# Kernel optimization log

Hardware: AMD Instinct MI355X
Metric: run time of the kernel (lower is better)

The kernel has to match this reference:

```python
import jax, jax.numpy as jnp
import numpy as np

NJ, NS = 30000, 12000            # num job / skill nodes
E_JS, E_SJ, E_SS = 300000, 300000, 150000
SBERT, HID, OUT = 384, 128, 128
H = 2                             # GAT heads (concat=True)
NEG_SLOPE = 0.2


def setup_inputs() -> dict:
    key = jax.random.key(0)
    ks = iter(jax.random.split(key, 64))
    nrm = lambda shape, s=1.0: jax.random.normal(next(ks), shape, jnp.float32) * s
    ridx = lambda n, hi: jax.random.randint(next(ks), (n,), 0, hi, jnp.int32)
    W = 0.05  # weight scale to keep activations sane across layers
    return dict(
        x_job=nrm((NJ, SBERT)), x_skill=nrm((NS, SBERT)),
        ei_js_src=ridx(E_JS, NJ), ei_js_dst=ridx(E_JS, NS),
        ei_sj_src=ridx(E_SJ, NS), ei_sj_dst=ridx(E_SJ, NJ),
        ei_ss_src=ridx(E_SS, NS), ei_ss_dst=ridx(E_SS, NS),
        query=nrm((SBERT,)),
        W0_job=nrm((SBERT, HID), W), b0_job=jnp.zeros((HID,), jnp.float32),
        g0_job=jnp.ones((HID,), jnp.float32), be0_job=jnp.zeros((HID,), jnp.float32),
        W0_skill=nrm((SBERT, HID), W), b0_skill=jnp.zeros((HID,), jnp.float32),
        g0_skill=jnp.ones((HID,), jnp.float32), be0_skill=jnp.zeros((HID,), jnp.float32),
        gat_Ws=nrm((2, 3, HID, H * HID), W), gat_Wd=nrm((2, 3, HID, H * HID), W),
        gat_as=nrm((2, 3, H, HID), W), gat_ad=nrm((2, 3, H, HID), W),
        gat_b=jnp.zeros((2, 3, H * HID), jnp.float32),
        inter_W=nrm((2, 2, H * HID, HID), W), inter_b=jnp.zeros((2, 2, HID), jnp.float32),
        Wjf=nrm((HID, OUT), W), bjf=jnp.zeros((OUT,), jnp.float32),
        Wq=nrm((SBERT, OUT), W), bq=jnp.zeros((OUT,), jnp.float32),
    )


def _layer_norm(x, g, b):
    mu = x.mean(-1, keepdims=True)
    var = ((x - mu) ** 2).mean(-1, keepdims=True)
    return (x - mu) * jax.lax.rsqrt(var + 1e-5) * g + b


def _gat(x_src, x_dst, src, dst, Ws, Wd, a_s, a_d, bias, num_dst):
    # PyG GATConv: lin_src/lin_dst (no bias), additive attention, scatter-softmax over dst.
    hs = (x_src @ Ws).reshape(-1, H, HID)            # [Ns,H,C]
    hd = (x_dst @ Wd).reshape(-1, H, HID)            # [Nd,H,C]
    e = jax.nn.leaky_relu((hs * a_s).sum(-1)[src] + (hd * a_d).sum(-1)[dst], NEG_SLOPE)  # [E,H]
    m = jax.ops.segment_max(e, dst, num_segments=num_dst)
    p = jnp.exp(e - m[dst])
    den = jax.ops.segment_sum(p, dst, num_segments=num_dst)
    w = p / (den[dst] + 1e-16)                       # [E,H]
    out = jax.ops.segment_sum(hs[src] * w[:, :, None], dst, num_segments=num_dst)
    return out.reshape(num_dst, H * HID) + bias


def _forward(x_job, x_skill, query,
             W0_job, b0_job, g0_job, be0_job, W0_skill, b0_skill, g0_skill, be0_skill,
             gat_Ws, gat_Wd, gat_as, gat_ad, gat_b, inter_W, inter_b, Wjf, bjf, Wq, bq,
             ei_js_src, ei_js_dst, ei_sj_src, ei_sj_dst, ei_ss_src, ei_ss_dst):
    # initial per-type lin + LN + relu (dropout = identity in eval)
    xj = jax.nn.relu(_layer_norm(x_job @ W0_job + b0_job, g0_job, be0_job))
    xs = jax.nn.relu(_layer_norm(x_skill @ W0_skill + b0_skill, g0_skill, be0_skill))
    # skill->skill relation adds self loops (src == dst node type)
    loops = jnp.arange(NS, dtype=jnp.int32)
    ss_src = jnp.concatenate([ei_ss_src, loops])
    ss_dst = jnp.concatenate([ei_ss_dst, loops])
    for i in range(2):  # num_layers
        o_s = (_gat(xj, xs, ei_js_src, ei_js_dst, gat_Ws[i, 0], gat_Wd[i, 0],
                    gat_as[i, 0], gat_ad[i, 0], gat_b[i, 0], NS)
               + _gat(xs, xs, ss_src, ss_dst, gat_Ws[i, 2], gat_Wd[i, 2],
                      gat_as[i, 2], gat_ad[i, 2], gat_b[i, 2], NS))  # HeteroConv aggr='sum'
        o_j = _gat(xs, xj, ei_sj_src, ei_sj_dst, gat_Ws[i, 1], gat_Wd[i, 1],
                   gat_as[i, 1], gat_ad[i, 1], gat_b[i, 1], NJ)
        xj = jax.nn.relu(o_j @ inter_W[i, 0] + inter_b[i, 0])
        xs = jax.nn.relu(o_s @ inter_W[i, 1] + inter_b[i, 1])
    job_emb = xj @ Wjf + bjf                          # [NJ,OUT]
    q = query @ Wq + bq                               # [OUT]
    scores = job_emb @ q                              # [NJ]
    return scores, job_emb, q


def reference(x_job, x_skill, ei_js_src, ei_js_dst, ei_sj_src, ei_sj_dst,
              ei_ss_src, ei_ss_dst, query,
              W0_job, b0_job, g0_job, be0_job, W0_skill, b0_skill, g0_skill, be0_skill,
              gat_Ws, gat_Wd, gat_as, gat_ad, gat_b, inter_W, inter_b,
              Wjf, bjf, Wq, bq):
    return _forward(x_job, x_skill, query,
                    W0_job, b0_job, g0_job, be0_job, W0_skill, b0_skill, g0_skill, be0_skill,
                    gat_Ws, gat_Wd, gat_as, gat_ad, gat_b, inter_W, inter_b, Wjf, bjf, Wq, bq,
                    ei_js_src, ei_js_dst, ei_sj_src, ei_sj_dst, ei_ss_src, ei_ss_dst)
```

## Files before the change

kernel.cpp:

```cpp
#include <hip/hip_runtime.h>
#include <hip/hip_bf16.h>
#include <math.h>

#define NJ 30000
#define NS 12000
#define E_JS 300000
#define E_SJ 300000
#define E_SS 150000
#define ETOT (E_JS + E_SJ + E_SS + NS)
#define NBINS (NS + NJ + NS)
#define NBUK ((NBINS + 63) / 64)
#define SBERT 384
#define HIST_NB 512
#define SCAT_NB 120
#define CAST_MATS 10
#define CAST_BPM 48
#define PREP_CAST (CAST_MATS * CAST_BPM)
#define PREP_WA   (PREP_CAST + 12)
#define PREP_QV   PREP_WA
#define PREP_HIST (PREP_QV + 1)

static inline int cdiv(int a, int b) { return (a + b - 1) / b; }

typedef __attribute__((ext_vector_type(8))) short bf8_t;
typedef __attribute__((ext_vector_type(4))) float f4_t;
typedef unsigned short u16;

__device__ inline float bf2f(unsigned short u) {
    union { unsigned int i; float f; } z; z.i = ((unsigned int)u) << 16; return z.f;
}
__device__ inline unsigned short f2bf(float f) {
    unsigned int x = __float_as_uint(f);
    unsigned int r = (x + 0x7fffu + ((x >> 16) & 1u)) >> 16;
    return (unsigned short)r;
}

__device__ inline void edge_decode(int e, const int* js_src, const int* js_dst,
                                   const int* sj_src, const int* sj_dst,
                                   const int* ss_src, const int* ss_dst,
                                   int& src, int& bin) {
    if (e < E_JS) { src = js_src[e]; bin = js_dst[e]; }
    else if (e < E_JS + E_SJ) { int i = e - E_JS; src = sj_src[i]; bin = NS + sj_dst[i]; }
    else if (e < E_JS + E_SJ + E_SS) { int i = e - E_JS - E_SJ; src = ss_src[i]; bin = NS + NJ + ss_dst[i]; }
    else { int i = e - E_JS - E_SJ - E_SS; src = i; bin = NS + NJ + i; }
}

struct CastT { const float* src; unsigned short* dst; int K; int N; };
struct PrepArgs {
    CastT m[CAST_MATS];
    const float* Ws; const float* as_; const float* Wd; const float* ad_;
    float* wsa; float* wda; int* bcnt;
    const float* query; const float* Wq; const float* bq; float* qv;
    const int* js_src; const int* js_dst;
    const int* sj_src; const int* sj_dst;
    const int* ss_src; const int* ss_dst;
};

__global__ __launch_bounds__(256) void k_prep(PrepArgs A) {
    __shared__ float ldt[32][33];
    __shared__ int lh[NBUK];
    int b = blockIdx.x;
    if (b < PREP_CAST) {
        int mi = b / CAST_BPM, bx = b % CAST_BPM;
        CastT cm = A.m[mi];
        int tilesN = cm.N >> 5;
        int total = (cm.K >> 5) * tilesN;
        if (bx >= total) return;
        int tk = bx / tilesN, tn = bx % tilesN;
        int k0 = tk * 32, n0 = tn * 32;
        int col = threadIdx.x & 31;
        int row0 = threadIdx.x >> 5;
#pragma unroll
        for (int r = 0; r < 4; ++r) {
            int kk = row0 + r * 8;
            ldt[kk][col] = cm.src[(size_t)(k0 + kk) * cm.N + n0 + col];
        }
        __syncthreads();
#pragma unroll
        for (int r = 0; r < 4; ++r) {
            int nn = row0 + r * 8;
            cm.dst[(size_t)(n0 + nn) * cm.K + k0 + col] = f2bf(ldt[col][nn]);
        }
    } else if (b < PREP_WA) {
        int id = (b - PREP_CAST) * 256 + threadIdx.x;
        if (id >= 2 * 1536) return;
        int which = id / 1536;
        int r = id % 1536;
        int lr = r / 256;
        int kh = r % 256;
        int k = kh / 2, h = kh % 2;
        const float* W = which ? A.Wd : A.Ws;
        const float* a = which ? A.ad_ : A.as_;
        const float* wrow = W + ((size_t)(lr * 128 + k)) * 256 + h * 128;
        const float* arow = a + (size_t)(lr * 2 + h) * 128;
        float acc = 0.f;
        for (int c2 = 0; c2 < 128; ++c2) acc += wrow[c2] * arow[c2];
        (which ? A.wda : A.wsa)[lr * 256 + k * 2 + h] = acc;
    } else if (b == PREP_QV) {
        int c = threadIdx.x;
        if (c < 128) {
            float acc = A.bq[c];
            for (int k = 0; k < SBERT; ++k) acc += A.query[k] * A.Wq[(size_t)k * 128 + c];
            A.qv[c] = acc;
        }
    } else {
        int t = threadIdx.x;
        for (int i = t; i < NBUK; i += 256) lh[i] = 0;
        __syncthreads();
        int hb = b - PREP_HIST;
        for (int e = hb * 256 + t; e < ETOT; e += HIST_NB * 256) {
            int src, bin;
            edge_decode(e, A.js_src, A.js_dst, A.sj_src, A.sj_dst, A.ss_src, A.ss_dst, src, bin);
            atomicAdd(&lh[bin >> 6], 1);
        }
        __syncthreads();
        for (int i = t; i < NBUK; i += 256) {
            int v = lh[i];
            if (v) atomicAdd(&A.bcnt[i], v);
        }
    }
}

struct GJob {
    const void* X; const unsigned short* Wt;
    const float* bias; const float* gamma; const float* beta;
    void* Y; int M; int K; int N; int ldY; int srcf32;
    const float* qv; float* sc;
    int aMode = 0;
    const float* wav0 = nullptr; const float* wav1 = nullptr;
    const float* wav2 = nullptr; const float* wav3 = nullptr;
    float* aOut = nullptr; int aStride = 0;
};
struct GPair { GJob a; GJob b; int blocksA; };

template <int EPI>
__device__ void mgemm_body(const GPair& P, int bx, int by) {
    int mb = bx;
    GJob g = (mb < P.blocksA) ? P.a : P.b;
    if (mb >= P.blocksA) mb -= P.blocksA;
    const int n0 = by * 128;
    if (n0 >= g.N) return;
    const int row0 = mb * 64;

    __shared__ __align__(16) unsigned short Al[64][40];
    __shared__ __align__(16) unsigned short Bl[128][40];
    const int t = threadIdx.x;
    const int wave = t >> 6, lane = t & 63;
    const int q = lane >> 4, c = lane & 15;
    const int K = g.K;

    f4_t acc[8];
#pragma unroll
    for (int nt = 0; nt < 8; ++nt) acc[nt] = (f4_t){0.f, 0.f, 0.f, 0.f};

    for (int k0 = 0; k0 < K; k0 += 32) {
#pragma unroll
        for (int it = 0; it < 3; ++it) {
            int idx = t + it * 256;
            int r = idx >> 2, cc = (idx & 3) * 8;
            if (r < 64) {
                int gr = row0 + r;
                if (g.srcf32) {
                    ushort4 lo = make_ushort4(0, 0, 0, 0), hi = lo;
                    if (gr < g.M) {
                        const float* Xf = (const float*)g.X;
                        const float* p = &Xf[(size_t)gr * K + k0 + cc];
                        float4 f0 = *(const float4*)p;
                        float4 f1 = *(const float4*)(p + 4);
                        lo = make_ushort4(f2bf(f0.x), f2bf(f0.y), f2bf(f0.z), f2bf(f0.w));
                        hi = make_ushort4(f2bf(f1.x), f2bf(f1.y), f2bf(f1.z), f2bf(f1.w));
                    }
                    *(ushort4*)&Al[r][cc] = lo;
                    *(ushort4*)&Al[r][cc + 4] = hi;
                } else {
                    const unsigned short* Xb = (const unsigned short*)g.X;
                    uint4 va = (gr < g.M) ? *(const uint4*)&Xb[(size_t)gr * K + k0 + cc]
                                          : make_uint4(0u, 0u, 0u, 0u);
                    *(uint4*)&Al[r][cc] = va;
                }
            } else {
                int br = r - 64;
                *(uint4*)&Bl[br][cc] = *(const uint4*)&g.Wt[(size_t)(n0 + br) * K + k0 + cc];
            }
        }
        __syncthreads();
        bf8_t af = *(const bf8_t*)&Al[wave * 16 + c][q * 8];
#pragma unroll
        for (int nt = 0; nt < 8; ++nt) {
            bf8_t bfr = *(const bf8_t*)&Bl[nt * 16 + c][q * 8];
            acc[nt] = __builtin_amdgcn_mfma_f32_16x16x32_bf16(af, bfr, acc[nt], 0, 0, 0);
        }
        __syncthreads();
    }

    float bcol[8], gcol[8], becol[8], qcol[8];
#pragma unroll
    for (int nt = 0; nt < 8; ++nt) {
        bcol[nt] = (EPI >= 1) ? g.bias[n0 + nt * 16 + c] : 0.f;
        if constexpr (EPI == 3) {
            gcol[nt] = g.gamma[nt * 16 + c];
            becol[nt] = g.beta[nt * 16 + c];
        }
        if constexpr (EPI == 1) qcol[nt] = g.qv[n0 + nt * 16 + c];
    }

#pragma unroll
    for (int r = 0; r < 4; ++r) {
        int grow = row0 + wave * 16 + q * 4 + r;
        float v[8];
#pragma unroll
        for (int nt = 0; nt < 8; ++nt) v[nt] = acc[nt][r] + bcol[nt];
        if constexpr (EPI == 3) {
            float s = 0.f, ss = 0.f;
#pragma unroll
            for (int nt = 0; nt < 8; ++nt) { s += v[nt]; ss += v[nt] * v[nt]; }
#pragma unroll
            for (int m = 8; m >= 1; m >>= 1) {
                s += __shfl_xor(s, m, 64);
                ss += __shfl_xor(ss, m, 64);
            }
            float mu = s * (1.f / 128.f);
            float var = ss * (1.f / 128.f) - mu * mu;
            float rs = rsqrtf(var + 1e-5f);
#pragma unroll
            for (int nt = 0; nt < 8; ++nt)
                v[nt] = fmaxf((v[nt] - mu) * rs * gcol[nt] + becol[nt], 0.f);
        } else if constexpr (EPI == 2) {
#pragma unroll
            for (int nt = 0; nt < 8; ++nt) v[nt] = fmaxf(v[nt], 0.f);
        }
        if constexpr (EPI == 1) {
            float part = 0.f;
#pragma unroll
            for (int nt = 0; nt < 8; ++nt) part += v[nt] * qcol[nt];
#pragma unroll
            for (int m = 8; m >= 1; m >>= 1) part += __shfl_xor(part, m, 64);
            if (c == 0 && grow < g.M) g.sc[grow] = part;
        }
        if (g.aMode > 0) {
            float pa[8];
#pragma unroll
            for (int i = 0; i < 8; ++i) pa[i] = 0.f;
#pragma unroll
            for (int nt = 0; nt < 8; ++nt) {
                int col = nt * 16 + c;
                float2 w0 = *(const float2*)&g.wav0[col * 2];
                pa[0] += v[nt] * w0.x; pa[1] += v[nt] * w0.y;
                if (g.aMode > 1) {
                    float2 w1 = *(const float2*)&g.wav1[col * 2];
                    pa[2] += v[nt] * w1.x; pa[3] += v[nt] * w1.y;
                }
                if (g.aMode > 2) {
                    float2 w2 = *(const float2*)&g.wav2[col * 2];
                    float2 w3 = *(const float2*)&g.wav3[col * 2];
                    pa[4] += v[nt] * w2.x; pa[5] += v[nt] * w2.y;
                    pa[6] += v[nt] * w3.x; pa[7] += v[nt] * w3.y;
                }
            }
#pragma unroll
            for (int m = 8; m >= 1; m >>= 1) {
                pa[0] += __shfl_xor(pa[0], m, 64); pa[1] += __shfl_xor(pa[1], m, 64);
                pa[2] += __shfl_xor(pa[2], m, 64); pa[3] += __shfl_xor(pa[3], m, 64);
                pa[4] += __shfl_xor(pa[4], m, 64); pa[5] += __shfl_xor(pa[5], m, 64);
                pa[6] += __shfl_xor(pa[6], m, 64); pa[7] += __shfl_xor(pa[7], m, 64);
            }
            if (c == 0 && grow < g.M) {
                float* ao = &g.aOut[(size_t)grow * g.aStride];
                ao[0] = pa[0]; ao[1] = pa[1];
                if (g.aMode > 1) { ao[2] = pa[2]; ao[3] = pa[3]; }
                if (g.aMode > 2) { ao[4] = pa[4]; ao[5] = pa[5]; ao[6] = pa[6]; ao[7] = pa[7]; }
            }
        }
        if (grow < g.M) {
            if constexpr (EPI == 1) {
                float* Y = (float*)g.Y;
#pragma unroll
                for (int nt = 0; nt < 8; ++nt)
                    Y[(size_t)grow * g.ldY + n0 + nt * 16 + c] = v[nt];
            } else {
                unsigned short* Y = (unsigned short*)g.Y;
#pragma unroll
                for (int nt = 0; nt < 8; ++nt)
                    Y[(size_t)grow * g.ldY + n0 + nt * 16 + c] = f2bf(v[nt]);
            }
        }
    }
}

template <int EPI>
__global__ __launch_bounds__(256) void k_mgemm(GPair P) {
    mgemm_body<EPI>(P, blockIdx.x, blockIdx.y);
}

__global__ __launch_bounds__(256) void k_lin0_scan(
    GPair P, int gemmBlocks,
    const int* __restrict__ bcnt, int* __restrict__ bukoff, int* __restrict__ bukcur) {
    if (blockIdx.x < (unsigned)gemmBlocks) {
        mgemm_body<3>(P, blockIdx.x, 0);
        return;
    }
    __shared__ int sd[256];
    int t = threadIdx.x;
    int i0 = t * 4;
    int v0 = (i0 < NBUK) ? bcnt[i0] : 0;
    int v1 = (i0 + 1 < NBUK) ? bcnt[i0 + 1] : 0;
    int v2 = (i0 + 2 < NBUK) ? bcnt[i0 + 2] : 0;
    int v3 = (i0 + 3 < NBUK) ? bcnt[i0 + 3] : 0;
    int csum = v0 + v1 + v2 + v3;
    sd[t] = csum;
    __syncthreads();
    for (int off = 1; off < 256; off <<= 1) {
        int tmp = (t >= off) ? sd[t - off] : 0;
        __syncthreads();
        sd[t] += tmp;
        __syncthreads();
    }
    int excl = sd[t] - csum;
    int p0 = excl, p1 = excl + v0, p2 = excl + v0 + v1, p3 = excl + v0 + v1 + v2;
    if (i0 < NBUK) { bukoff[i0] = p0; bukcur[i0] = p0; }
    if (i0 + 1 < NBUK) { bukoff[i0 + 1] = p1; bukcur[i0 + 1] = p1; }
    if (i0 + 2 < NBUK) { bukoff[i0 + 2] = p2; bukcur[i0 + 2] = p2; }
    if (i0 + 3 < NBUK) { bukoff[i0 + 3] = p3; bukcur[i0 + 3] = p3; }
    if (t == 0) bukoff[NBUK] = ETOT;
}

__global__ __launch_bounds__(256) void k_scatter_proj(
    GPair P, int gemmBlocks,
    const int* __restrict__ js_src, const int* __restrict__ js_dst,
    const int* __restrict__ sj_src, const int* __restrict__ sj_dst,
    const int* __restrict__ ss_src, const int* __restrict__ ss_dst,
    int* __restrict__ bukcur, uint2* __restrict__ pairs) {
    if (blockIdx.x < (unsigned)gemmBlocks) {
        mgemm_body<0>(P, blockIdx.x, blockIdx.y);
        return;
    }
    if (blockIdx.y != 0) return;
    __shared__ int lh[NBUK];
    __shared__ int lbase[NBUK];
    int t = threadIdx.x;
    int sb = blockIdx.x - gemmBlocks;
    const int CH = (ETOT + SCAT_NB - 1) / SCAT_NB;
    const int beg = sb * CH;
    const int endi = (beg + CH < ETOT) ? beg + CH : ETOT;
    for (int i = t; i < NBUK; i += 256) lh[i] = 0;
    __syncthreads();
    for (int e = beg + t; e < endi; e += 256) {
        int src, bin;
        edge_decode(e, js_src, js_dst, sj_src, sj_dst, ss_src, ss_dst, src, bin);
        atomicAdd(&lh[bin >> 6], 1);
    }
    __syncthreads();
    for (int i = t; i < NBUK; i += 256) {
        int v = lh[i];
        lbase[i] = v ? atomicAdd(&bukcur[i], v) : 0;
    }
    __syncthreads();
    for (int i = t; i < NBUK; i += 256) lh[i] = 0;
    __syncthreads();
    for (int e = beg + t; e < endi; e += 256) {
        int src, bin;
        edge_decode(e, js_src, js_dst, sj_src, sj_dst, ss_src, ss_dst, src, bin);
        int bu = bin >> 6;
        int pos = lbase[bu] + atomicAdd(&lh[bu], 1);
        pairs[pos] = make_uint2((unsigned)src, (unsigned)bin);
    }
}

__global__ __launch_bounds__(256) void k_finalize(
    const uint2* __restrict__ pairs, const int* __restrict__ bukoff,
    int* __restrict__ offs, int* __restrict__ esrc) {
    int b = blockIdx.x, t = threadIdx.x;
    int base = bukoff[b], endi = bukoff[b + 1];
    __shared__ int cnt[64], excl[64], curs[64];
    if (t < 64) cnt[t] = 0;
    __syncthreads();
    for (int i = base + t; i < endi; i += 256)
        atomicAdd(&cnt[pairs[i].y & 63], 1);
    __syncthreads();
    if (t < 64) {
        int v = cnt[t];
        int inc = v;
#pragma unroll
        for (int off = 1; off < 64; off <<= 1) {
            int tmp = __shfl_up(inc, off, 64);
            if (t >= off) inc += tmp;
        }
        excl[t] = inc - v;
        curs[t] = inc - v;
    }
    __syncthreads();
    for (int i = base + t; i < endi; i += 256) {
        uint2 p = pairs[i];
        int lb = p.y & 63;
        int pos = atomicAdd(&curs[lb], 1);
        esrc[base + pos] = (int)p.x;
    }
    if (t < 64) {
        int bin = b * 64 + t;
        if (bin < NBINS) offs[bin] = base + excl[t];
    }
    if (b == 0 && t == 0) offs[NBINS] = ETOT;
}

__device__ inline void edge_accum(
    const int* __restrict__ esrc, int beg, int endi,
    const float* __restrict__ aSrc, int sStride, int hOff, float ad,
    const unsigned short* __restrict__ hs, int hsLd, int c,
    float& ax, float& ay, float& az, float& aw, float& den) {
    for (int j = beg; j < endi; j += 4) {
        int j1 = j + 1 < endi ? j + 1 : endi - 1;
        int j2 = j + 2 < endi ? j + 2 : endi - 1;
        int j3 = j + 3 < endi ? j + 3 : endi - 1;
        int s0 = esrc[j], s1 = esrc[j1], s2 = esrc[j2], s3 = esrc[j3];
        float as0 = aSrc[(size_t)s0 * sStride + hOff];
        float as1 = aSrc[(size_t)s1 * sStride + hOff];
        float as2 = aSrc[(size_t)s2 * sStride + hOff];
        float as3 = aSrc[(size_t)s3 * sStride + hOff];
        ushort4 v0 = *(const ushort4*)&hs[(size_t)s0 * hsLd + c];
        ushort4 v1 = *(const ushort4*)&hs[(size_t)s1 * hsLd + c];
        ushort4 v2 = *(const ushort4*)&hs[(size_t)s2 * hsLd + c];
        ushort4 v3 = *(const ushort4*)&hs[(size_t)s3 * hsLd + c];
        float e0 = as0 + ad; e0 = e0 > 0.f ? e0 : 0.2f * e0;
        float e1 = as1 + ad; e1 = e1 > 0.f ? e1 : 0.2f * e1;
        float e2 = as2 + ad; e2 = e2 > 0.f ? e2 : 0.2f * e2;
        float e3 = as3 + ad; e3 = e3 > 0.f ? e3 : 0.2f * e3;
        float p0 = __expf(e0);
        float p1 = (j + 1 < endi) ? __expf(e1) : 0.f;
        float p2 = (j + 2 < endi) ? __expf(e2) : 0.f;
        float p3 = (j + 3 < endi) ? __expf(e3) : 0.f;
        ax += p0 * bf2f(v0.x) + p1 * bf2f(v1.x) + p2 * bf2f(v2.x) + p3 * bf2f(v3.x);
        ay += p0 * bf2f(v0.y) + p1 * bf2f(v1.y) + p2 * bf2f(v2.y) + p3 * bf2f(v3.y);
        az += p0 * bf2f(v0.z) + p1 * bf2f(v1.z) + p2 * bf2f(v2.z) + p3 * bf2f(v3.z);
        aw += p0 * bf2f(v0.w) + p1 * bf2f(v1.w) + p2 * bf2f(v2.w) + p3 * bf2f(v3.w);
        den += p0 + p1 + p2 + p3;
    }
}

__global__ __launch_bounds__(256) void k_gather_all(
    const int* __restrict__ offs, const int* __restrict__ esrc,
    const float* __restrict__ aJ, const float* __restrict__ aS,
    const unsigned short* __restrict__ hs1,
    const unsigned short* __restrict__ hsss, int ssLd,
    const unsigned short* __restrict__ hsj, int sjLd,
    const float* __restrict__ gb,
    unsigned short* __restrict__ oj, unsigned short* __restrict__ os,
    int jobOnly) {
    int wave = threadIdx.x >> 6, lane = threadIdx.x & 63;
    int idx = blockIdx.x * 4 + wave;
    int c = lane * 4;
    int h = (c >= 128) ? 1 : 0;
    if (jobOnly) {
        if (idx >= NJ) return;
        int d = idx;
        float ax = 0.f, ay = 0.f, az = 0.f, aw = 0.f, den = 0.f;
        int bb = NS + d;
        edge_accum(esrc, offs[bb], offs[bb + 1], aS, 8, 4 + h, aJ[(size_t)d * 4 + 2 + h],
                   hsj, sjLd, c, ax, ay, az, aw, den);
        float sc = 1.f / (den + 1e-16f);
        float4 b4 = *(const float4*)&gb[256 + c];
        float o0 = ax * sc + b4.x, o1 = ay * sc + b4.y;
        float o2 = az * sc + b4.z, o3 = aw * sc + b4.w;
        ushort4 o; o.x = f2bf(o0); o.y = f2bf(o1); o.z = f2bf(o2); o.w = f2bf(o3);
        *(ushort4*)&oj[(size_t)d * 256 + c] = o;
        return;
    }
    if (idx < NS) {
        int d = idx;
        float axA = 0.f, ayA = 0.f, azA = 0.f, awA = 0.f, denA = 0.f;
        edge_accum(esrc, offs[d], offs[d + 1], aJ, 4, h, aS[(size_t)d * 8 + 2 + h],
                   hs1, 256, c, axA, ayA, azA, awA, denA);
        float axB = 0.f, ayB = 0.f, azB = 0.f, awB = 0.f, denB = 0.f;
        int bb = NS + NJ + d;
        edge_accum(esrc, offs[bb], offs[bb + 1], aS, 8, h, aS[(size_t)d * 8 + 6 + h],
                   hsss, ssLd, c, axB, ayB, azB, awB, denB);
        float scA = 1.f / (denA + 1e-16f);
        float scB = 1.f / (denB + 1e-16f);
        float4 bA = *(const float4*)&gb[c];
        float4 bB = *(const float4*)&gb[512 + c];
        float o0 = axA * scA + bA.x + axB * scB + bB.x;
        float o1 = ayA * scA + bA.y + ayB * scB + bB.y;
        float o2 = azA * scA + bA.z + azB * scB + bB.z;
        float o3 = awA * scA + bA.w + awB * scB + bB.w;
        ushort4 o; o.x = f2bf(o0); o.y = f2bf(o1); o.z = f2bf(o2); o.w = f2bf(o3);
        *(ushort4*)&os[(size_t)d * 256 + c] = o;
    } else if (idx < NS + NJ) {
        int d = idx - NS;
        float ax = 0.f, ay = 0.f, az = 0.f, aw = 0.f, den = 0.f;
        int bb = NS + d;
        edge_accum(esrc, offs[bb], offs[bb + 1], aS, 8, 4 + h, aJ[(size_t)d * 4 + 2 + h],
                   hsj, sjLd, c, ax, ay, az, aw, den);
        float sc = 1.f / (den + 1e-16f);
        float4 b4 = *(const float4*)&gb[256 + c];
        float o0 = ax * sc + b4.x, o1 = ay * sc + b4.y;
        float o2 = az * sc + b4.z, o3 = aw * sc + b4.w;
        ushort4 o; o.x = f2bf(o0); o.y = f2bf(o1); o.z = f2bf(o2); o.w = f2bf(o3);
        *(ushort4*)&oj[(size_t)d * 256 + c] = o;
    }
}

struct FJob {
    const unsigned short* X; const unsigned short* Wt1; const float* bias1;
    int M; int K1;
    const float* wa; float* aOut; int aStride;
    const unsigned short* Wt2; const float* bias2; int N2;
    void* Y2; int ldY2; int y2f32;
    const float* qv; float* sc;
};
struct FPair { FJob a; FJob b; int blocksA; };

__global__ __launch_bounds__(256) void k_fused2(FPair P) {
    int mb = blockIdx.x;
    FJob g = (mb < P.blocksA) ? P.a : P.b;
    if (mb >= P.blocksA) mb -= P.blocksA;
    const int row0 = mb * 64;

    __shared__ __align__(16) unsigned short Al[64][40];
    __shared__ __align__(16) unsigned short Bl[128][40];
    __shared__ __align__(16) unsigned short Y1l[4][64][40];
    const int t = threadIdx.x;
    const int wave = t >> 6, lane = t & 63;
    const int q = lane >> 4, c = lane & 15;

    f4_t acc[8];
#pragma unroll
    for (int nt = 0; nt < 8; ++nt) acc[nt] = (f4_t){0.f, 0.f, 0.f, 0.f};

    for (int k0 = 0; k0 < g.K1; k0 += 32) {
#pragma unroll
        for (int it = 0; it < 3; ++it) {
            int idx = t + it * 256;
            int r = idx >> 2, cc = (idx & 3) * 8;
            if (r < 64) {
                int gr = row0 + r;
                uint4 va = (gr < g.M) ? *(const uint4*)&g.X[(size_t)gr * g.K1 + k0 + cc]
                                      : make_uint4(0u, 0u, 0u, 0u);
                *(uint4*)&Al[r][cc] = va;
            } else {
                int br = r - 64;
                *(uint4*)&Bl[br][cc] = *(const uint4*)&g.Wt1[(size_t)br * g.K1 + k0 + cc];
            }
        }
        __syncthreads();
        bf8_t af = *(const bf8_t*)&Al[wave * 16 + c][q * 8];
#pragma unroll
        for (int nt = 0; nt < 8; ++nt) {
            bf8_t bfr = *(const bf8_t*)&Bl[nt * 16 + c][q * 8];
            acc[nt] = __builtin_amdgcn_mfma_f32_16x16x32_bf16(af, bfr, acc[nt], 0, 0, 0);
        }
        __syncthreads();
    }

    float bcol[8];
#pragma unroll
    for (int nt = 0; nt < 8; ++nt) bcol[nt] = g.bias1[nt * 16 + c];
#pragma unroll
    for (int r = 0; r < 4; ++r) {
        int row = wave * 16 + q * 4 + r;
        int grow = row0 + row;
        float v[8];
#pragma unroll
        for (int nt = 0; nt < 8; ++nt) v[nt] = fmaxf(acc[nt][r] + bcol[nt], 0.f);
        if (g.wa) {
            float pa0 = 0.f, pa1 = 0.f;
#pragma unroll
            for (int nt = 0; nt < 8; ++nt) {
                float2 w0 = *(const float2*)&g.wa[(nt * 16 + c) * 2];
                pa0 += v[nt] * w0.x; pa1 += v[nt] * w0.y;
            }
#pragma unroll
            for (int m = 8; m >= 1; m >>= 1) {
                pa0 += __shfl_xor(pa0, m, 64);
                pa1 += __shfl_xor(pa1, m, 64);
            }
            if (c == 0 && grow < g.M) {
                g.aOut[(size_t)grow * g.aStride + 0] = pa0;
                g.aOut[(size_t)grow * g.aStride + 1] = pa1;
            }
        }
#pragma unroll
        for (int nt = 0; nt < 8; ++nt)
            Y1l[nt >> 1][row][(nt & 1) * 16 + c] = f2bf(v[nt]);
    }
    if (g.N2 == 0) return;
    __syncthreads();

    for (int n2 = 0; n2 < g.N2; n2 += 128) {
        f4_t acc2[8];
#pragma unroll
        for (int nt = 0; nt < 8; ++nt) acc2[nt] = (f4_t){0.f, 0.f, 0.f, 0.f};
        for (int k0 = 0; k0 < 128; k0 += 32) {
#pragma unroll
            for (int it = 0; it < 2; ++it) {
                int idx = t + it * 256;
                int br = idx >> 2, cc = (idx & 3) * 8;
                *(uint4*)&Bl[br][cc] = *(const uint4*)&g.Wt2[(size_t)(n2 + br) * 128 + k0 + cc];
            }
            __syncthreads();
            bf8_t af = *(const bf8_t*)&Y1l[k0 >> 5][wave * 16 + c][q * 8];
#pragma unroll
            for (int nt = 0; nt < 8; ++nt) {
                bf8_t bfr = *(const bf8_t*)&Bl[nt * 16 + c][q * 8];
                acc2[nt] = __builtin_amdgcn_mfma_f32_16x16x32_bf16(af, bfr, acc2[nt], 0, 0, 0);
            }
            __syncthreads();
        }
        float b2[8], qcol[8];
#pragma unroll
        for (int nt = 0; nt < 8; ++nt) {
            b2[nt] = g.bias2 ? g.bias2[n2 + nt * 16 + c] : 0.f;
            if (g.y2f32) qcol[nt] = g.qv[n2 + nt * 16 + c];
        }
#pragma unroll
        for (int r = 0; r < 4; ++r) {
            int grow = row0 + wave * 16 + q * 4 + r;
            float v[8];
#pragma unroll
            for (int nt = 0; nt < 8; ++nt) v[nt] = acc2[nt][r] + b2[nt];
            if (g.y2f32) {
                float part = 0.f;
#pragma unroll
                for (int nt = 0; nt < 8; ++nt) part += v[nt] * qcol[nt];
#pragma unroll
                for (int m = 8; m >= 1; m >>= 1) part += __shfl_xor(part, m, 64);
                if (c == 0 && grow < g.M) g.sc[grow] = part;
                if (grow < g.M) {
                    float* Y = (float*)g.Y2;
#pragma unroll
                    for (int nt = 0; nt < 8; ++nt)
                        Y[(size_t)grow * g.ldY2 + n2 + nt * 16 + c] = v[nt];
                }
            } else if (grow < g.M) {
                unsigned short* Y = (unsigned short*)g.Y2;
#pragma unroll
                for (int nt = 0; nt < 8; ++nt)
                    Y[(size_t)grow * g.ldY2 + n2 + nt * 16 + c] = f2bf(v[nt]);
            }
        }
    }
}

extern "C" void kernel_launch(void* const* d_in, const int* in_sizes, int n_in,
                              void* d_out, int out_size, void* d_ws, size_t ws_size,
                              hipStream_t stream) {
    const float* x_job   = (const float*)d_in[0];
    const float* x_skill = (const float*)d_in[1];
    const int* js_src = (const int*)d_in[2];
    const int* js_dst = (const int*)d_in[3];
    const int* sj_src = (const int*)d_in[4];
    const int* sj_dst = (const int*)d_in[5];
    const int* ss_src = (const int*)d_in[6];
    const int* ss_dst = (const int*)d_in[7];
    const float* query    = (const float*)d_in[8];
    const float* W0_job   = (const float*)d_in[9];
    const float* b0_job   = (const float*)d_in[10];
    const float* g0_job   = (const float*)d_in[11];
    const float* be0_job  = (const float*)d_in[12];
    const float* W0_skill = (const float*)d_in[13];
    const float* b0_skill = (const float*)d_in[14];
    const float* g0_skill = (const float*)d_in[15];
    const float* be0_skill= (const float*)d_in[16];
    const float* gat_Ws = (const float*)d_in[17];
    const float* gat_Wd = (const float*)d_in[18];
    const float* gat_as = (const float*)d_in[19];
    const float* gat_ad = (const float*)d_in[20];
    const float* gat_b  = (const float*)d_in[21];
    const float* inter_W = (const float*)d_in[22];
    const float* inter_b = (const float*)d_in[23];
    const float* Wjf = (const float*)d_in[24];
    const float* bjf = (const float*)d_in[25];
    const float* Wq  = (const float*)d_in[26];
    const float* bq  = (const float*)d_in[27];

    char* w = (char*)d_ws;
    auto alloc = [&](size_t bytes) -> void* {
        void* p = (void*)w;
        w += (bytes + 255) & ~(size_t)255;
        return p;
    };
    u16* xj  = (u16*)alloc((size_t)NJ * 128 * 2);
    u16* xs  = (u16*)alloc((size_t)NS * 128 * 2);
    u16* hs1 = (u16*)alloc((size_t)NJ * 256 * 2);
    u16* hs2 = (u16*)alloc((size_t)NS * 512 * 2);
    u16* hs3 = (u16*)alloc((size_t)NS * 256 * 2);
    u16* oj  = (u16*)alloc((size_t)NJ * 256 * 2);
    u16* os  = (u16*)alloc((size_t)NS * 256 * 2);
    u16* WtW0j = (u16*)alloc((size_t)SBERT * 128 * 2);
    u16* WtW0s = (u16*)alloc((size_t)SBERT * 128 * 2);
    u16* WtWs  = (u16*)alloc((size_t)6 * 128 * 256 * 2);
    u16* WtI   = (u16*)alloc((size_t)4 * 256 * 128 * 2);
    u16* WtJf  = (u16*)alloc((size_t)128 * 128 * 2);
    float* aJ = (float*)alloc((size_t)NJ * 4 * 4);
    float* aS = (float*)alloc((size_t)NS * 8 * 4);
    float* wsa = (float*)alloc(6 * 256 * 4);
    float* wda = (float*)alloc(6 * 256 * 4);
    int* bcnt   = (int*)alloc((size_t)NBUK * 4);
    int* bukoff = (int*)alloc((size_t)(NBUK + 1) * 4);
    int* bukcur = (int*)alloc((size_t)NBUK * 4);
    uint2* pairs = (uint2*)alloc((size_t)ETOT * 8);
    int* offs = (int*)alloc((size_t)(NBINS + 1) * 4);
    int* esrc = (int*)alloc((size_t)ETOT * 4);

    float* out = (float*)d_out;
    float* scores  = out;
    float* job_emb = out + NJ;
    float* qv      = out + NJ + (size_t)NJ * 128;

    const int mbJ = cdiv(NJ, 64);
    const int mbS = cdiv(NS, 64);
    const int gemmB = mbJ + mbS;

    hipMemsetAsync(bcnt, 0, (size_t)NBUK * 4, stream);

    {
        PrepArgs A;
        A.m[0] = {W0_job, WtW0j, SBERT, 128};
        A.m[1] = {W0_skill, WtW0s, SBERT, 128};
        A.m[2] = {gat_Ws + (size_t)0 * 128 * 256, WtWs + (size_t)0 * 256 * 128, 128, 256};
        A.m[3] = {gat_Ws + (size_t)1 * 128 * 256, WtWs + (size_t)1 * 256 * 128, 128, 256};
        A.m[4] = {gat_Ws + (size_t)2 * 128 * 256, WtWs + (size_t)2 * 256 * 128, 128, 256};
        A.m[5] = {gat_Ws + (size_t)4 * 128 * 256, WtWs + (size_t)4 * 256 * 128, 128, 256};
        A.m[6] = {inter_W + (size_t)0 * 256 * 128, WtI + (size_t)0 * 128 * 256, 256, 128};
        A.m[7] = {inter_W + (size_t)1 * 256 * 128, WtI + (size_t)1 * 128 * 256, 256, 128};
        A.m[8] = {inter_W + (size_t)2 * 256 * 128, WtI + (size_t)2 * 128 * 256, 256, 128};
        A.m[9] = {Wjf, WtJf, 128, 128};
        A.Ws = gat_Ws; A.as_ = gat_as; A.Wd = gat_Wd; A.ad_ = gat_ad;
        A.wsa = wsa; A.wda = wda; A.bcnt = bcnt;
        A.query = query; A.Wq = Wq; A.bq = bq; A.qv = qv;
        A.js_src = js_src; A.js_dst = js_dst;
        A.sj_src = sj_src; A.sj_dst = sj_dst;
        A.ss_src = ss_src; A.ss_dst = ss_dst;
        k_prep<<<PREP_HIST + HIST_NB, 256, 0, stream>>>(A);
    }

    {
        GPair P;
        P.a = {x_job, WtW0j, b0_job, g0_job, be0_job, xj, NJ, SBERT, 128, 128, 1,
               nullptr, nullptr, 2, wsa + 0, wda + 256, nullptr, nullptr, aJ, 4};
        P.b = {x_skill, WtW0s, b0_skill, g0_skill, be0_skill, xs, NS, SBERT, 128, 128, 1,
               nullptr, nullptr, 4, wsa + 2 * 256, wda + 0, wsa + 1 * 256, wda + 2 * 256, aS, 8};
        P.blocksA = mbJ;
        k_lin0_scan<<<dim3(gemmB + 1, 1), 256, 0, stream>>>(P, gemmB, bcnt, bukoff, bukcur);
    }

    {
        GPair P;
        P.a = {xj, WtWs + (size_t)0 * 256 * 128, nullptr, nullptr, nullptr,
               hs1, NJ, 128, 256, 256, 0, nullptr, nullptr};
        P.b = {xs, WtWs + (size_t)1 * 256 * 128, nullptr, nullptr, nullptr,
               hs2, NS, 128, 512, 512, 0, nullptr, nullptr};
        P.blocksA = mbJ;
        k_scatter_proj<<<dim3(gemmB + SCAT_NB, 4), 256, 0, stream>>>(
            P, gemmB, js_src, js_dst, sj_src, sj_dst, ss_src, ss_dst, bukcur, pairs);
    }

    k_finalize<<<NBUK, 256, 0, stream>>>(pairs, bukoff, offs, esrc);

    k_gather_all<<<cdiv(NS + NJ, 4), 256, 0, stream>>>(
        offs, esrc, aJ, aS, hs1, hs2 + 256, 512, hs2, 512, gat_b, oj, os, 0);

    {
        FPair P;
        P.a = {oj, WtI + (size_t)0 * 128 * 256, inter_b + 0, NJ, 256,
               wda + (size_t)4 * 256, aJ + 2, 4,
               nullptr, nullptr, 0, nullptr, 0, 0, nullptr, nullptr};
        P.b = {os, WtI + (size_t)1 * 128 * 256, inter_b + 128, NS, 256,
               wsa + (size_t)4 * 256, aS + 4, 8,
               WtWs + (size_t)4 * 256 * 128, nullptr, 256, hs3, 256, 0, nullptr, nullptr};
        P.blocksA = mbJ;
        k_fused2<<<dim3(gemmB, 1), 256, 0, stream>>>(P);
    }

    k_gather_all<<<cdiv(NJ, 4), 256, 0, stream>>>(
        offs, esrc, aJ, aS, nullptr, nullptr, 0, hs3, 256,
        gat_b + (size_t)3 * 256, oj, nullptr, 1);

    {
        FPair P;
        P.a = {oj, WtI + (size_t)2 * 128 * 256, inter_b + 2 * 128, NJ, 256,
               nullptr, nullptr, 0,
               WtJf, bjf, 128, job_emb, 128, 1, qv, scores};
        P.b = P.a;
        P.blocksA = mbJ;
        k_fused2<<<dim3(mbJ, 1), 256, 0, stream>>>(P);
    }
}
```

Baseline: 344.3 us.

## Split gather wave into two edge halves with 16-byte row loads

The GAT edge-aggregation kernel now splits each wavefront into two 32-lane halves. Each half processes alternate edges of the destination and loads 8 bf16 columns (16 bytes) per lane instead of 4, and the halves are combined with a cross-lane shuffle before normalization. This doubles the edges in flight per wave and widens each global load, aiming to hide gather latency. It also replaces stride multiplies with shifts and uses bit-shift bf16 unpacking. The cost is extra shuffle reductions and duplicated attention-score loads per edge across both heads' lanes.

```diff
diff --git a/kernel.cpp b/kernel.cpp
--- a/kernel.cpp
+++ b/kernel.cpp
@@ -402,99 +402,155 @@
     if (b == 0 && t == 0) offs[NBINS] = ETOT;
 }
 
-__device__ inline void edge_accum(
-    const int* __restrict__ esrc, int beg, int endi,
-    const float* __restrict__ aSrc, int sStride, int hOff, float ad,
-    const unsigned short* __restrict__ hs, int hsLd, int c,
-    float& ax, float& ay, float& az, float& aw, float& den) {
-    for (int j = beg; j < endi; j += 4) {
-        int j1 = j + 1 < endi ? j + 1 : endi - 1;
-        int j2 = j + 2 < endi ? j + 2 : endi - 1;
-        int j3 = j + 3 < endi ? j + 3 : endi - 1;
-        int s0 = esrc[j], s1 = esrc[j1], s2 = esrc[j2], s3 = esrc[j3];
-        float as0 = aSrc[(size_t)s0 * sStride + hOff];
-        float as1 = aSrc[(size_t)s1 * sStride + hOff];
-        float as2 = aSrc[(size_t)s2 * sStride + hOff];
-        float as3 = aSrc[(size_t)s3 * sStride + hOff];
-        ushort4 v0 = *(const ushort4*)&hs[(size_t)s0 * hsLd + c];
-        ushort4 v1 = *(const ushort4*)&hs[(size_t)s1 * hsLd + c];
-        ushort4 v2 = *(const ushort4*)&hs[(size_t)s2 * hsLd + c];
-        ushort4 v3 = *(const ushort4*)&hs[(size_t)s3 * hsLd + c];
-        float e0 = as0 + ad; e0 = e0 > 0.f ? e0 : 0.2f * e0;
-        float e1 = as1 + ad; e1 = e1 > 0.f ? e1 : 0.2f * e1;
-        float e2 = as2 + ad; e2 = e2 > 0.f ? e2 : 0.2f * e2;
-        float e3 = as3 + ad; e3 = e3 > 0.f ? e3 : 0.2f * e3;
-        float p0 = __expf(e0);
-        float p1 = (j + 1 < endi) ? __expf(e1) : 0.f;
-        float p2 = (j + 2 < endi) ? __expf(e2) : 0.f;
-        float p3 = (j + 3 < endi) ? __expf(e3) : 0.f;
-        ax += p0 * bf2f(v0.x) + p1 * bf2f(v1.x) + p2 * bf2f(v2.x) + p3 * bf2f(v3.x);
-        ay += p0 * bf2f(v0.y) + p1 * bf2f(v1.y) + p2 * bf2f(v2.y) + p3 * bf2f(v3.y);
-        az += p0 * bf2f(v0.z) + p1 * bf2f(v1.z) + p2 * bf2f(v2.z) + p3 * bf2f(v3.z);
-        aw += p0 * bf2f(v0.w) + p1 * bf2f(v1.w) + p2 * bf2f(v2.w) + p3 * bf2f(v3.w);
-        den += p0 + p1 + p2 + p3;
-    }
+__device__ inline void fmacc8(float p, uint4 u, float acc[8]) {
+    acc[0] += p * __uint_as_float(u.x << 16);
+    acc[1] += p * __uint_as_float(u.x & 0xffff0000u);
+    acc[2] += p * __uint_as_float(u.y << 16);
+    acc[3] += p * __uint_as_float(u.y & 0xffff0000u);
+    acc[4] += p * __uint_as_float(u.z << 16);
+    acc[5] += p * __uint_as_float(u.z & 0xffff0000u);
+    acc[6] += p * __uint_as_float(u.w << 16);
+    acc[7] += p * __uint_as_float(u.w & 0xffff0000u);
+}
+
+__device__ inline void rel_run(
+    const int* __restrict__ esrc, int beg, int cnt,
+    const float* __restrict__ aSrc, int aShift, int aOff, float ad,
+    const unsigned short* __restrict__ hs, int ldShift, int colBase, int half,
+    float acc[8], float& den) {
+    int n2 = cnt & ~1;
+    int j = beg;
+    for (; j + 4 <= beg + n2; j += 4) {
+        int sA = esrc[j + half];
+        int sB = esrc[j + 2 + half];
+        uint4 uA = *(const uint4*)&hs[((size_t)sA << ldShift) + colBase];
+        uint4 uB = *(const uint4*)&hs[((size_t)sB << ldShift) + colBase];
+        float aA = aSrc[((size_t)sA << aShift) + aOff];
+        float aB = aSrc[((size_t)sB << aShift) + aOff];
+        float eA = aA + ad; eA = eA > 0.f ? eA : 0.2f * eA;
+        float eB = aB + ad; eB = eB > 0.f ? eB : 0.2f * eB;
+        float pA = __expf(eA), pB = __expf(eB);
+        fmacc8(pA, uA, acc);
+        fmacc8(pB, uB, acc);
+        den += pA + pB;
+    }
+    for (; j < beg + n2; j += 2) {
+        int s = esrc[j + half];
+        uint4 u = *(const uint4*)&hs[((size_t)s << ldShift) + colBase];
+        float a = aSrc[((size_t)s << aShift) + aOff];
+        float e = a + ad; e = e > 0.f ? e : 0.2f * e;
+        float p = __expf(e);
+        fmacc8(p, u, acc);
+        den += p;
+    }
+    if (cnt & 1) {
+        if (!half) {
+            int s = esrc[beg + cnt - 1];
+            uint4 u = *(const uint4*)&hs[((size_t)s << ldShift) + colBase];
+            float a = aSrc[((size_t)s << aShift) + aOff];
+            float e = a + ad; e = e > 0.f ? e : 0.2f * e;
+            float p = __expf(e);
+            fmacc8(p, u, acc);
+            den += p;
+        }
+    }
+}
+
+__device__ inline void reduce_scale(float acc[8], float& den, float out[8], int add) {
+    float d = den + __shfl_xor(den, 32, 64);
+    float sc = 1.f / (d + 1e-16f);
+#pragma unroll
+    for (int i = 0; i < 8; ++i) {
+        float t = acc[i] + __shfl_xor(acc[i], 32, 64);
+        if (add) out[i] += t * sc; else out[i] = t * sc;
+    }
+}
+
+__device__ inline void store8(unsigned short* dst, const float v[8]) {
+    uint4 o;
+    o.x = (unsigned)f2bf(v[0]) | ((unsigned)f2bf(v[1]) << 16);
+    o.y = (unsigned)f2bf(v[2]) | ((unsigned)f2bf(v[3]) << 16);
+    o.z = (unsigned)f2bf(v[4]) | ((unsigned)f2bf(v[5]) << 16);
+    o.w = (unsigned)f2bf(v[6]) | ((unsigned)f2bf(v[7]) << 16);
+    *(uint4*)dst = o;
 }
 
 __global__ __launch_bounds__(256) void k_gather_all(
     const int* __restrict__ offs, const int* __restrict__ esrc,
     const float* __restrict__ aJ, const float* __restrict__ aS,
     const unsigned short* __restrict__ hs1,
-    const unsigned short* __restrict__ hsss, int ssLd,
-    const unsigned short* __restrict__ hsj, int sjLd,
+    const unsigned short* __restrict__ hsss, int ssShift,
+    const unsigned short* __restrict__ hsj, int sjShift,
     const float* __restrict__ gb,
     unsigned short* __restrict__ oj, unsigned short* __restrict__ os,
     int jobOnly) {
     int wave = threadIdx.x >> 6, lane = threadIdx.x & 63;
     int idx = blockIdx.x * 4 + wave;
-    int c = lane * 4;
-    int h = (c >= 128) ? 1 : 0;
+    int half = lane >> 5;
+    int colBase = (lane & 31) * 8;
+    int myH = (colBase >= 128) ? 1 : 0;
+
+    float acc[8], den, out[8];
+#pragma unroll
+    for (int i = 0; i < 8; ++i) acc[i] = 0.f;
+    den = 0.f;
+
     if (jobOnly) {
         if (idx >= NJ) return;
         int d = idx;
-        float ax = 0.f, ay = 0.f, az = 0.f, aw = 0.f, den = 0.f;
         int bb = NS + d;
-        edge_accum(esrc, offs[bb], offs[bb + 1], aS, 8, 4 + h, aJ[(size_t)d * 4 + 2 + h],
-                   hsj, sjLd, c, ax, ay, az, aw, den);
-        float sc = 1.f / (den + 1e-16f);
-        float4 b4 = *(const float4*)&gb[256 + c];
-        float o0 = ax * sc + b4.x, o1 = ay * sc + b4.y;
-        float o2 = az * sc + b4.z, o3 = aw * sc + b4.w;
-        ushort4 o; o.x = f2bf(o0); o.y = f2bf(o1); o.z = f2bf(o2); o.w = f2bf(o3);
-        *(ushort4*)&oj[(size_t)d * 256 + c] = o;
+        int beg = offs[bb], cnt = offs[bb + 1] - beg;
+        float ad = aJ[(size_t)d * 4 + 2 + myH];
+        rel_run(esrc, beg, cnt, aS, 3, 4 + myH, ad, hsj, sjShift, colBase, half, acc, den);
+        reduce_scale(acc, den, out, 0);
+        if (half == 0) {
+            float4 b0 = *(const float4*)&gb[256 + colBase];
+            float4 b1 = *(const float4*)&gb[256 + colBase + 4];
+            out[0] += b0.x; out[1] += b0.y; out[2] += b0.z; out[3] += b0.w;
+            out[4] += b1.x; out[5] += b1.y; out[6] += b1.z; out[7] += b1.w;
+            store8(&oj[(size_t)d * 256 + colBase], out);
+        }
         return;
     }
     if (idx < NS) {
         int d = idx;
-        float axA = 0.f, ayA = 0.f, azA = 0.f, awA = 0.f, denA = 0.f;
-        edge_accum(esrc, offs[d], offs[d + 1], aJ, 4, h, aS[(size_t)d * 8 + 2 + h],
-                   hs1, 256, c, axA, ayA, azA, awA, denA);
-        float axB = 0.f, ayB = 0.f, azB = 0.f, awB = 0.f, denB = 0.f;
+        int beg = offs[d], cnt = offs[d + 1] - beg;
+        float adA = aS[(size_t)d * 8 + 2 + myH];
+        rel_run(esrc, beg, cnt, aJ, 2, myH, adA, hs1, 8, colBase, half, acc, den);
+        reduce_scale(acc, den, out, 0);
+#pragma unroll
+        for (int i = 0; i < 8; ++i) acc[i] = 0.f;
+        den = 0.f;
         int bb = NS + NJ + d;
-        edge_accum(esrc, offs[bb], offs[bb + 1], aS, 8, h, aS[(size_t)d * 8 + 6 + h],
-                   hsss, ssLd, c, axB, ayB, azB, awB, denB);
-        float scA = 1.f / (denA + 1e-16f);
-        float scB = 1.f / (denB + 1e-16f);
-        float4 bA = *(const float4*)&gb[c];
-        float4 bB = *(const float4*)&gb[512 + c];
-        float o0 = axA * scA + bA.x + axB * scB + bB.x;
-        float o1 = ayA * scA + bA.y + ayB * scB + bB.y;
-        float o2 = azA * scA + bA.z + azB * scB + bB.z;
-        float o3 = awA * scA + bA.w + awB * scB + bB.w;
-        ushort4 o; o.x = f2bf(o0); o.y = f2bf(o1); o.z = f2bf(o2); o.w = f2bf(o3);
-        *(ushort4*)&os[(size_t)d * 256 + c] = o;
+        int beg2 = offs[bb], cnt2 = offs[bb + 1] - beg2;
+        float adB = aS[(size_t)d * 8 + 6 + myH];
+        rel_run(esrc, beg2, cnt2, aS, 3, myH, adB, hsss, ssShift, colBase, half, acc, den);
+        reduce_scale(acc, den, out, 1);
+        if (half == 0) {
+            float4 bA0 = *(const float4*)&gb[colBase];
+            float4 bA1 = *(const float4*)&gb[colBase + 4];
+            float4 bB0 = *(const float4*)&gb[512 + colBase];
+            float4 bB1 = *(const float4*)&gb[512 + colBase + 4];
+            out[0] += bA0.x + bB0.x; out[1] += bA0.y + bB0.y;
+            out[2] += bA0.z + bB0.z; out[3] += bA0.w + bB0.w;
+            out[4] += bA1.x + bB1.x; out[5] += bA1.y + bB1.y;
+            out[6] += bA1.z + bB1.z; out[7] += bA1.w + bB1.w;
+            store8(&os[(size_t)d * 256 + colBase], out);
+        }
     } else if (idx < NS + NJ) {
         int d = idx - NS;
-        float ax = 0.f, ay = 0.f, az = 0.f, aw = 0.f, den = 0.f;
         int bb = NS + d;
-        edge_accum(esrc, offs[bb], offs[bb + 1], aS, 8, 4 + h, aJ[(size_t)d * 4 + 2 + h],
-                   hsj, sjLd, c, ax, ay, az, aw, den);
-        float sc = 1.f / (den + 1e-16f);
-        float4 b4 = *(const float4*)&gb[256 + c];
-        float o0 = ax * sc + b4.x, o1 = ay * sc + b4.y;
-        float o2 = az * sc + b4.z, o3 = aw * sc + b4.w;
-        ushort4 o; o.x = f2bf(o0); o.y = f2bf(o1); o.z = f2bf(o2); o.w = f2bf(o3);
-        *(ushort4*)&oj[(size_t)d * 256 + c] = o;
+        int beg = offs[bb], cnt = offs[bb + 1] - beg;
+        float ad = aJ[(size_t)d * 4 + 2 + myH];
+        rel_run(esrc, beg, cnt, aS, 3, 4 + myH, ad, hsj, sjShift, colBase, half, acc, den);
+        reduce_scale(acc, den, out, 0);
+        if (half == 0) {
+            float4 b0 = *(const float4*)&gb[256 + colBase];
+            float4 b1 = *(const float4*)&gb[256 + colBase + 4];
+            out[0] += b0.x; out[1] += b0.y; out[2] += b0.z; out[3] += b0.w;
+            out[4] += b1.x; out[5] += b1.y; out[6] += b1.z; out[7] += b1.w;
+            store8(&oj[(size_t)d * 256 + colBase], out);
+        }
     }
 }
 
@@ -756,7 +812,7 @@
     k_finalize<<<NBUK, 256, 0, stream>>>(pairs, bukoff, offs, esrc);
 
     k_gather_all<<<cdiv(NS + NJ, 4), 256, 0, stream>>>(
-        offs, esrc, aJ, aS, hs1, hs2 + 256, 512, hs2, 512, gat_b, oj, os, 0);
+        offs, esrc, aJ, aS, hs1, hs2 + 256, 9, hs2, 9, gat_b, oj, os, 0);
 
     {
         FPair P;
@@ -771,7 +827,7 @@
     }
 
     k_gather_all<<<cdiv(NJ, 4), 256, 0, stream>>>(
-        offs, esrc, aJ, aS, nullptr, nullptr, 0, hs3, 256,
+        offs, esrc, aJ, aS, nullptr, nullptr, 8, hs3, 8,
         gat_b + (size_t)3 * 256, oj, nullptr, 1);
 
     {
```

Result: no change. 339.3 us (median of 2 runs) (-1.4%).
